# Kernel optimization log

Measured on AMD Instinct MI355X. Metric: run time of the kernel, lower is better.

Reference implementation:

```python
import jax, jax.numpy as jnp
import numpy as np

V, E, U, D, B, T = 32000, 256, 512, 512, 32, 64


def setup_inputs() -> dict:
    key = jax.random.key(0)
    ks = jax.random.split(key, 12)
    g = lambda k, shape: (jax.random.normal(k, shape, jnp.float32) * 0.05)
    return dict(
        x=jax.random.randint(ks[0], (B, T), 0, V),
        emb=g(ks[1], (V, E)),
        Wxf=g(ks[2], (E, 4 * U)), Whf=g(ks[3], (U, 4 * U)), bf=jnp.zeros((4 * U,), jnp.float32),
        Wxb=g(ks[4], (E, 4 * U)), Whb=g(ks[5], (U, 4 * U)), bb=jnp.zeros((4 * U,), jnp.float32),
        W1=g(ks[6], (2 * U + D, 10)), b1=jnp.zeros((10,), jnp.float32),
        W2=g(ks[7], (10, 1)), b2=jnp.zeros((1,), jnp.float32),
        Wxd=g(ks[8], (2 * U, 4 * D)), Whd=g(ks[9], (D, 4 * D)), bd=jnp.zeros((4 * D,), jnp.float32),
        Wo=g(ks[10], (D, V)), bo=jnp.zeros((V,), jnp.float32),
    )


def lstm_cell(x_t, h, c, Wx, Wh, b):
    # Keras gate order: i, f, g(cell), o
    z = x_t @ Wx + h @ Wh + b
    i, f, g, o = jnp.split(z, 4, axis=-1)
    c = jax.nn.sigmoid(f) * c + jax.nn.sigmoid(i) * jnp.tanh(g)
    h = jax.nn.sigmoid(o) * jnp.tanh(c)
    return h, c


def lstm_seq(xs, Wx, Wh, b):
    # xs: [T, B, F] -> hidden states [T, B, units]
    units = Wh.shape[0]
    h0 = jnp.zeros((xs.shape[1], units), xs.dtype)

    def step(carry, x_t):
        h, c = lstm_cell(x_t, carry[0], carry[1], Wx, Wh, b)
        return (h, c), h

    _, hs = jax.lax.scan(step, (h0, h0), xs)
    return hs


def reference(x, emb, Wxf, Whf, bf, Wxb, Whb, bb, W1, b1, W2, b2, Wxd, Whd, bd, Wo, bo):
    Bsz, Tlen = x.shape
    xe = emb[x]                              # [B, T, E]
    xs = jnp.swapaxes(xe, 0, 1)              # [T, B, E]
    hf = lstm_seq(xs, Wxf, Whf, bf)          # forward direction
    hb = lstm_seq(xs[::-1], Wxb, Whb, bb)[::-1]  # backward direction
    a = jnp.swapaxes(jnp.concatenate([hf, hb], axis=-1), 0, 1)  # [B, T, 2U]
    du = Whd.shape[0]

    def dec_step(carry, _):
        h, c = carry
        s_rep = jnp.broadcast_to(h[:, None, :], (Bsz, Tlen, du))
        cat = jnp.concatenate([a, s_rep], axis=-1)              # [B, T, 2U+D]
        e = jax.nn.relu(jnp.tanh(cat @ W1 + b1) @ W2 + b2)      # [B, T, 1]
        score = jax.nn.softmax(e, axis=1)
        ctx = jnp.sum(score * a, axis=1)                        # [B, 2U]
        h, c = lstm_cell(ctx, h, c, Wxd, Whd, bd)
        out = jax.nn.softmax(h @ Wo + bo, axis=-1)              # [B, V]
        return (h, c), out

    init = (jnp.zeros((Bsz, du), a.dtype), jnp.zeros((Bsz, du), a.dtype))
    _, outs = jax.lax.scan(dec_step, init, None, length=Tlen)
    return jnp.swapaxes(outs, 0, 1)  # [B, T, V]
```

## Files before the change

kernel.cpp:

```cpp
#include <hip/hip_runtime.h>
#include <hip/hip_bf16.h>
#include <cstdint>

typedef float f32x4 __attribute__((ext_vector_type(4)));
typedef __bf16 bf16x8 __attribute__((ext_vector_type(8)));

__device__ __forceinline__ uint32_t bf1(float x) {
  uint32_t u = __float_as_uint(x);
  return (u + 0x7fffu + ((u >> 16) & 1u)) >> 16;
}
__device__ __forceinline__ uint32_t bpack(float lo, float hi) {
  return bf1(lo) | (bf1(hi) << 16);
}
__device__ __forceinline__ float blo(uint32_t u) { return __uint_as_float(u << 16); }
__device__ __forceinline__ float bhi(uint32_t u) { return __uint_as_float(u & 0xffff0000u); }
__device__ __forceinline__ float sigm(float x) {
  return __fdividef(1.f, 1.f + exp2f(x * -1.4426950408889634f));
}
__device__ __forceinline__ float tanhf_fast(float x) {
  float e2 = exp2f(x * 2.8853900817779268f);
  return 1.f - __fdividef(2.f, e2 + 1.f);
}

__device__ __forceinline__ float dot2bf(uint32_t a, uint32_t b, float acc) {
  asm("v_dot2_f32_bf16 %0, %1, %2, %0" : "+v"(acc) : "v"(a), "v"(b));
  return acc;
}

#define GLOAD_LDS16(g, l)                                                     \
  __builtin_amdgcn_global_load_lds(                                           \
      (const __attribute__((address_space(1))) void*)(g),                     \
      (__attribute__((address_space(3))) void*)(l), 16, 0, 0)
#define GLOAD_LDS4(g, l)                                                      \
  __builtin_amdgcn_global_load_lds(                                           \
      (const __attribute__((address_space(1))) void*)(g),                     \
      (__attribute__((address_space(3))) void*)(l), 4, 0, 0)

__global__ __launch_bounds__(256) void k0_pack(
    const float* __restrict__ Whf, const float* __restrict__ Whb,
    uint32_t* __restrict__ Wencp, const float* __restrict__ Whd,
    uint32_t* __restrict__ Wdp, const float* __restrict__ W1,
    uint32_t* __restrict__ W1pbAll)
{
  int bid = blockIdx.x;
  if (bid < 4096) {
    int p = bid * 256 + threadIdx.x;
    int j2 = p & 3, slot = (p >> 2) & 63, c = (p >> 8) & 15;
    int cg = (p >> 12) & 127, dir = p >> 19;
    int k = slot * 8 + j2 * 2;
    const float* W = dir ? Whb : Whf;
    int colg = (c >> 2) * 512 + cg * 4 + (c & 3);
    Wencp[p ^ ((c & 7) << 2)] =
        bpack(W[(size_t)k * 2048 + colg], W[(size_t)(k + 1) * 2048 + colg]);
  } else if (bid < 6144) {
    int p = (bid - 4096) * 256 + threadIdx.x;
    int e = p & 3, cc = (p >> 2) & 31, q4 = (p >> 7) & 63, ug = p >> 13;
    int k2 = 4 * q4 + e;
    int col = (cc >> 3) * 512 + ug * 8 + (cc & 7);
    int k = 2 * k2;
    Wdp[p] = bpack(Whd[(size_t)k * 2048 + col], Whd[(size_t)(k + 1) * 2048 + col]);
  } else {
    int p = (bid - 6144) * 256 + threadIdx.x;
    if (p < 9216) {
      int q = p / 12, j = p % 12;
      float v0 = (j < 10) ? W1[(size_t)(2 * q) * 10 + j] : 0.f;
      float v1 = (j < 10) ? W1[(size_t)(2 * q + 1) * 10 + j] : 0.f;
      W1pbAll[p] = bpack(v0, v1);
    }
  }
}

__global__ __launch_bounds__(256) void k_wT(
    const float* __restrict__ src, ushort* __restrict__ dst, int K, int N)
{
  __shared__ float tile[64 * 65];
  const int t = threadIdx.x;
  const int n0 = blockIdx.x * 64, k0 = blockIdx.y * 64;
  for (int i = 0; i < 16; ++i) {
    int p = t + 256 * i;
    int kk = p >> 6, nn = p & 63;
    tile[kk * 65 + nn] = src[(size_t)(k0 + kk) * N + n0 + nn];
  }
  __syncthreads();
  for (int i = 0; i < 4; ++i) {
    int p = t + 256 * i;
    int nn = p >> 4, k4 = (p & 15) * 4;
    ushort4 o;
    o.x = (ushort)bf1(tile[(k4 + 0) * 65 + nn]);
    o.y = (ushort)bf1(tile[(k4 + 1) * 65 + nn]);
    o.z = (ushort)bf1(tile[(k4 + 2) * 65 + nn]);
    o.w = (ushort)bf1(tile[(k4 + 3) * 65 + nn]);
    *(ushort4*)(dst + (size_t)(n0 + nn) * K + k0 + k4) = o;
  }
}

__global__ __launch_bounds__(256) void k1_embed_mfma(
    const int* __restrict__ x, const float* __restrict__ emb,
    const ushort* __restrict__ WxfT, const ushort* __restrict__ WxbT,
    const float* __restrict__ bfv, const float* __restrict__ bbv,
    float* __restrict__ Xf, float* __restrict__ Xb)
{
  __shared__ float Afp[128 * 64];
  __shared__ ushort Bs[128 * 64];
  __shared__ int xid[128];
  const int t = threadIdx.x;
  const int n0g = blockIdx.x * 128;
  const int m0 = blockIdx.y * 128;
  const int isB = (n0g >= 2048);
  const int n0 = n0g & 2047;
  const ushort* WT = isB ? WxbT : WxfT;
  const float* bias = isB ? bbv : bfv;
  if (t < 128) xid[t] = x[m0 + t];
  __syncthreads();
  int xr[8];
#pragma unroll
  for (int i = 0; i < 8; ++i) xr[i] = xid[(t >> 4) + 16 * i];
  const int lane = t & 63, w = t >> 6;
  const int quad = lane >> 4, l15 = lane & 15;
  f32x4 acc[2][8] = {};
  for (int kc = 0; kc < 4; ++kc) {
    const int k0 = kc * 64;
    __syncthreads();
    for (int i = 0; i < 8; ++i) {
      int idx = t + 256 * i;
      int row = (t >> 4) + 16 * i, ch = idx & 15;
      int gr = (ch >> 1) ^ (row & 7), w16 = ch & 1;
      GLOAD_LDS16(emb + (size_t)xr[i] * 256 + k0 + gr * 8 + w16 * 4,
                  Afp + idx * 4);
    }
    for (int i = 0; i < 4; ++i) {
      int idx = t + 256 * i;
      int row = idx >> 3, s8 = (idx & 7) ^ (row & 7);
      GLOAD_LDS16(WT + (size_t)(n0 + row) * 256 + k0 + s8 * 8,
                  Bs + idx * 8);
    }
    __syncthreads();
#pragma unroll
    for (int ks = 0; ks < 2; ++ks) {
      int kq = ks * 4 + quad;
      bf16x8 af[2];
#pragma unroll
      for (int mi = 0; mi < 2; ++mi) {
        int row = w * 32 + mi * 16 + l15;
        int slot = kq ^ (row & 7);
        const float* ap = Afp + row * 64 + slot * 8;
        float4 a0 = *(const float4*)ap;
        float4 a1 = *(const float4*)(ap + 4);
        union { ushort u[8]; bf16x8 v; } cv;
        cv.u[0] = (ushort)bf1(a0.x); cv.u[1] = (ushort)bf1(a0.y);
        cv.u[2] = (ushort)bf1(a0.z); cv.u[3] = (ushort)bf1(a0.w);
        cv.u[4] = (ushort)bf1(a1.x); cv.u[5] = (ushort)bf1(a1.y);
        cv.u[6] = (ushort)bf1(a1.z); cv.u[7] = (ushort)bf1(a1.w);
        af[mi] = cv.v;
      }
#pragma unroll
      for (int ni = 0; ni < 8; ++ni) {
        int rowB = ni * 16 + l15;
        int slotB = kq ^ (rowB & 7);
        bf16x8 bfr = *(const bf16x8*)(Bs + rowB * 64 + slotB * 8);
#pragma unroll
        for (int mi = 0; mi < 2; ++mi)
          acc[mi][ni] = __builtin_amdgcn_mfma_f32_16x16x32_bf16(
              af[mi], bfr, acc[mi][ni], 0, 0, 0);
      }
    }
  }
  float* Xout = isB ? Xb : Xf;
  float bcol[8];
#pragma unroll
  for (int ni = 0; ni < 8; ++ni) bcol[ni] = bias[n0 + ni * 16 + l15];
#pragma unroll
  for (int mi = 0; mi < 2; ++mi) {
#pragma unroll
    for (int reg = 0; reg < 4; ++reg) {
      int token = m0 + w * 32 + mi * 16 + quad * 4 + reg;
#pragma unroll
      for (int ni = 0; ni < 8; ++ni) {
        int col = n0 + ni * 16 + l15;
        Xout[(size_t)token * 2048 + col] = acc[mi][ni][reg] + bcol[ni];
      }
    }
  }
}

__global__ __launch_bounds__(256) void k2_enc_step(
    const float* __restrict__ Xf, const float* __restrict__ Xb,
    const uint32_t* __restrict__ Wencp,
    const uint32_t* __restrict__ hfi, uint32_t* __restrict__ hfo,
    const uint32_t* __restrict__ hbi, uint32_t* __restrict__ hbo,
    float* __restrict__ cf, float* __restrict__ cb,
    ushort* __restrict__ aB, int step)
{
  __shared__ ushort Hs[16 * 512];
  __shared__ ushort Ws[16 * 512];
  __shared__ float zp[4 * 256];
  __shared__ float zx[256];
  __shared__ float zbuf[256];
  __shared__ float hl[64];
  const int t = threadIdx.x;
  const int dir = blockIdx.x >> 8;
  const int rh = (blockIdx.x >> 7) & 1;
  const int cg = blockIdx.x & 127;
  const int r0 = rh * 16, u0 = cg * 4;
  const float* XF = dir ? Xb : Xf;
  const uint32_t* hin = dir ? hbi : hfi;
  uint32_t* hout = dir ? hbo : hfo;
  float* cst = dir ? cb : cf;
  const int ta = dir ? (63 - step) : step;

  {
    const uint32_t* hinu = hin + r0 * 256;
    for (int i = 0; i < 4; ++i) {
      int b4 = (t >> 6) * 64 + 256 * i;
      GLOAD_LDS16(hinu + (size_t)(t + 256 * i) * 4, (uint32_t*)Hs + b4 * 4);
    }
    const uint32_t* wsrc = Wencp + ((size_t)dir * 128 + cg) * 4096;
    for (int i = 0; i < 4; ++i) {
      int b4 = (t >> 6) * 64 + 256 * i;
      GLOAD_LDS16(wsrc + (size_t)(t + 256 * i) * 4, (uint32_t*)Ws + b4 * 4);
    }
  }
  {
    int cl = t & 15, rl = t >> 4;
    int colg = (cl >> 2) * 512 + u0 + (cl & 3);
    GLOAD_LDS4(XF + (size_t)((r0 + rl) * 64 + ta) * 2048 + colg,
               zx + (t >> 6) * 64);
  }
  __syncthreads();
  const int lane = t & 63, w = t >> 6;
  const int quad = lane >> 4, l15 = lane & 15;
  f32x4 acc = {};
#pragma unroll
  for (int mm = 0; mm < 4; ++mm) {
    int m = w * 4 + mm;
    int slot = m * 4 + quad;
    bf16x8 a = *(const bf16x8*)(Hs + l15 * 512 + (slot ^ (l15 & 7)) * 8);
    bf16x8 b = *(const bf16x8*)(Ws + l15 * 512 + (slot ^ (l15 & 7)) * 8);
    acc = __builtin_amdgcn_mfma_f32_16x16x32_bf16(a, b, acc, 0, 0, 0);
  }
#pragma unroll
  for (int reg = 0; reg < 4; ++reg)
    zp[w * 256 + (quad * 4 + reg) * 16 + l15] = acc[reg];
  __syncthreads();
  zbuf[t] = zp[t] + zp[256 + t] + zp[512 + t] + zp[768 + t] + zx[t];
  __syncthreads();
  if (t < 64) {
    int rl = t & 15, ui = t >> 4;
    int u = u0 + ui, r = r0 + rl;
    float zi = zbuf[rl * 16 + ui];
    float zf = zbuf[rl * 16 + 4 + ui];
    float zg = zbuf[rl * 16 + 8 + ui];
    float zo = zbuf[rl * 16 + 12 + ui];
    float cold = cst[u * 32 + r];
    float cn = sigm(zf) * cold + sigm(zi) * tanhf_fast(zg);
    float h = sigm(zo) * tanhf_fast(cn);
    cst[u * 32 + r] = cn;
    aB[((size_t)r * 64 + ta) * 1024 + dir * 512 + u] = (ushort)bf1(h);
    hl[rl * 4 + ui] = h;
  }
  __syncthreads();
  if (t < 16) {
    int r = r0 + t;
    uint32_t lo = bpack(hl[t * 4 + 0], hl[t * 4 + 1]);
    uint32_t hi = bpack(hl[t * 4 + 2], hl[t * 4 + 3]);
    uint32_t* dst = hout + r * 256 + (((cg >> 1) ^ (r & 7)) * 4) + (cg & 1) * 2;
    *(uint2*)dst = make_uint2(lo, hi);
  }
}

__global__ __launch_bounds__(256) void k5_aw1(
    const ushort* __restrict__ aB, const uint32_t* __restrict__ W1pbAll,
    const float* __restrict__ b1, float* __restrict__ aw1)
{
  __shared__ uint32_t ar[512];
  __shared__ float ps[16 * 17];
  const int t = threadIdx.x;
  const uint32_t* aBu = (const uint32_t*)aB;
  for (int m = blockIdx.x; m < 2048; m += gridDim.x) {
    __syncthreads();
    *(uint2*)(&ar[t * 2]) = *(const uint2*)(aBu + (size_t)m * 512 + t * 2);
    __syncthreads();
    int j = t & 15, part = t >> 4;
    int jj = j < 10 ? j : 0;
    float s = 0.f;
#pragma unroll 8
    for (int q = part * 32; q < part * 32 + 32; ++q)
      s = dot2bf(ar[q], W1pbAll[q * 12 + jj], s);
    ps[part * 17 + j] = s;
    __syncthreads();
    if (t < 16) {
      float sum = 0.f;
      if (t < 10) {
        for (int p = 0; p < 16; ++p) sum += ps[p * 17 + t];
        sum += b1[t];
      }
      aw1[m * 16 + t] = sum;
    }
  }
}

__global__ __launch_bounds__(256) void kA_aprime(
    const ushort* __restrict__ WxdT, const ushort* __restrict__ aB,
    uint32_t* __restrict__ ApTb)
{
  __shared__ ushort As[128 * 64];
  __shared__ ushort Bs[128 * 64];
  const int t = threadIdx.x;
  const int lane = t & 63, w = t >> 6;
  const int wr = w >> 1, wc = w & 1;
  const int m0 = blockIdx.y * 128, n0 = blockIdx.x * 128;
  const int lrow = lane >> 3, s = lane & 7;
  const int quad = lane >> 4, l15 = lane & 15;
  f32x4 acc[4][4] = {};
  for (int kc = 0; kc < 16; ++kc) {
    const int k0 = kc * 64;
    __syncthreads();
    for (int i = 0; i < 4; ++i) {
      int row = w * 32 + i * 8 + lrow;
      int k8 = s ^ (row & 7);
      GLOAD_LDS16(WxdT + (size_t)(m0 + row) * 1024 + k0 + k8 * 8,
                  As + (w * 32 + i * 8) * 64);
      GLOAD_LDS16(aB + (size_t)(n0 + row) * 1024 + k0 + k8 * 8,
                  Bs + (w * 32 + i * 8) * 64);
    }
    __syncthreads();
#pragma unroll
    for (int ks = 0; ks < 2; ++ks) {
      bf16x8 af[4], bfr[4];
      int kq = ks * 4 + quad;
#pragma unroll
      for (int mi = 0; mi < 4; ++mi) {
        int row = wr * 64 + mi * 16 + l15;
        int slot = kq ^ (row & 7);
        af[mi] = *(const bf16x8*)(As + row * 64 + slot * 8);
      }
#pragma unroll
      for (int ni = 0; ni < 4; ++ni) {
        int row = wc * 64 + ni * 16 + l15;
        int slot = kq ^ (row & 7);
        bfr[ni] = *(const bf16x8*)(Bs + row * 64 + slot * 8);
      }
#pragma unroll
      for (int mi = 0; mi < 4; ++mi)
#pragma unroll
        for (int ni = 0; ni < 4; ++ni)
          acc[mi][ni] = __builtin_amdgcn_mfma_f32_16x16x32_bf16(
              af[mi], bfr[ni], acc[mi][ni], 0, 0, 0);
    }
  }
#pragma unroll
  for (int mi = 0; mi < 4; ++mi) {
    int mbase = m0 + wr * 64 + mi * 16 + quad * 4;
#pragma unroll
    for (int reg = 0; reg < 4; ++reg) {
      int m = mbase + reg;
#pragma unroll
      for (int ni = 0; ni < 4; ++ni) {
        int n = n0 + wc * 64 + ni * 16 + l15;
        float v = acc[mi][ni][reg];
        float v2 = __shfl_xor(v, 1);
        if (!(l15 & 1))
          ApTb[(size_t)m * 1024 + (n >> 1)] = bpack(v, v2);
      }
    }
  }
}

__global__ __launch_bounds__(256) void k4_dec_step(
    const uint32_t* __restrict__ ApTb, const float* __restrict__ aw1,
    const uint32_t* __restrict__ W1pb, const float* __restrict__ W2,
    const float* __restrict__ b2, const uint32_t* __restrict__ hdp_in,
    const uint32_t* __restrict__ Wdp, const float* __restrict__ bd,
    uint32_t* __restrict__ hdp_out, float* __restrict__ cd,
    ushort* __restrict__ HsB, int step)
{
  __shared__ uint32_t W1s[256 * 12];
  __shared__ uint32_t hdT[1024];
  __shared__ uint32_t Wsp[8192];
  __shared__ float ph[64 * 4 * 12];
  __shared__ float hw1[4 * 12];
  __shared__ float esc[4 * 65];
  __shared__ uint32_t escp[4 * 33];
  __shared__ float pm[4 * 9];
  __shared__ float mrow[4], srow[4];
  __shared__ float w2s[12];
  __shared__ float zp[2][128];
  __shared__ float zbuf[4 * 33];
  __shared__ float hl[32];
  const int t = threadIdx.x;
  const int ug = blockIdx.x >> 3;
  const int rg = blockIdx.x & 7;
  const int u0 = ug * 8, r0 = rg * 4;
  for (int i = 0; i < 3; ++i) {
    int b4 = (t >> 6) * 64 + 256 * i;
    GLOAD_LDS16(W1pb + (size_t)(t + 256 * i) * 4, W1s + (size_t)b4 * 4);
  }
  {
    int q4 = t >> 2, rl0 = t & 3;
    int b4 = (t >> 6) * 64;
    GLOAD_LDS16(hdp_in + (size_t)(q4 * 32 + r0 + rl0) * 4, hdT + (size_t)b4 * 4);
  }
  if (t < 12) w2s[t] = (t < 10) ? W2[t] : 0.f;
  __syncthreads();
  {
    const uint32_t* wsrc = Wdp + (size_t)ug * 8192;
    for (int i = 0; i < 8; ++i) {
      int b4 = (t >> 6) * 64 + 256 * i;
      GLOAD_LDS16(wsrc + (size_t)(t + 256 * i) * 4, Wsp + (size_t)b4 * 4);
    }
  }
  {
    const int rl = t & 3, kp = t >> 2;
    const uint4* hd4 = (const uint4*)hdT;
    float acc[10] = {};
    {
      uint4 u4 = hd4[kp * 4 + rl];
      const uint32_t* w0 = &W1s[(4 * kp) * 12];
      const uint32_t* w1 = &W1s[(4 * kp + 1) * 12];
      const uint32_t* w2p = &W1s[(4 * kp + 2) * 12];
      const uint32_t* w3 = &W1s[(4 * kp + 3) * 12];
#pragma unroll
      for (int j = 0; j < 10; ++j) {
        acc[j] = dot2bf(u4.x, w0[j], acc[j]);
        acc[j] = dot2bf(u4.y, w1[j], acc[j]);
        acc[j] = dot2bf(u4.z, w2p[j], acc[j]);
        acc[j] = dot2bf(u4.w, w3[j], acc[j]);
      }
    }
#pragma unroll
    for (int j = 0; j < 10; ++j) ph[(kp * 4 + rl) * 12 + j] = acc[j];
  }
  __syncthreads();
  if (t < 40) {
    int rl = t / 10, j = t % 10;
    float s = 0.f;
#pragma unroll
    for (int p = 0; p < 64; ++p) s += ph[(p * 4 + rl) * 12 + j];
    hw1[rl * 12 + j] = s;
  }
  __syncthreads();
  const float b2v = b2[0];
  {
    int rl = t >> 6, tt = t & 63;
    size_t m = (size_t)(r0 + rl) * 64 + tt;
    const float4* aw = (const float4*)(aw1 + m * 16);
    float4 q0 = aw[0], q1 = aw[1], q2 = aw[2];
    const float* hw = &hw1[rl * 12];
    float e = b2v;
    e += tanhf_fast(q0.x + hw[0]) * w2s[0];
    e += tanhf_fast(q0.y + hw[1]) * w2s[1];
    e += tanhf_fast(q0.z + hw[2]) * w2s[2];
    e += tanhf_fast(q0.w + hw[3]) * w2s[3];
    e += tanhf_fast(q1.x + hw[4]) * w2s[4];
    e += tanhf_fast(q1.y + hw[5]) * w2s[5];
    e += tanhf_fast(q1.z + hw[6]) * w2s[6];
    e += tanhf_fast(q1.w + hw[7]) * w2s[7];
    e += tanhf_fast(q2.x + hw[8]) * w2s[8];
    e += tanhf_fast(q2.y + hw[9]) * w2s[9];
    esc[rl * 65 + tt] = fmaxf(e, 0.f);
  }
  __syncthreads();
  if (t < 32) {
    int rl = t >> 3, part = t & 7;
    float m = -1e30f;
    for (int i = 0; i < 8; ++i) m = fmaxf(m, esc[rl * 65 + part * 8 + i]);
    pm[rl * 9 + part] = m;
  }
  __syncthreads();
  if (t < 4) {
    float m = pm[t * 9];
    for (int p = 1; p < 8; ++p) m = fmaxf(m, pm[t * 9 + p]);
    mrow[t] = m;
  }
  __syncthreads();
  if (t < 32) {
    int rl = t >> 3, part = t & 7;
    float m = mrow[rl];
    float s = 0.f;
    for (int i = 0; i < 8; ++i) s += __expf(esc[rl * 65 + part * 8 + i] - m);
    pm[rl * 9 + part] = s;
  }
  __syncthreads();
  if (t < 4) {
    float s = 0.f;
    for (int p = 0; p < 8; ++p) s += pm[t * 9 + p];
    srow[t] = __fdividef(1.f, s);
  }
  __syncthreads();
  if (t < 128) {
    int rl = t >> 5, q = t & 31;
    float m = mrow[rl], s = srow[rl];
    float v0 = __expf(esc[rl * 65 + 2 * q] - m) * s;
    float v1 = __expf(esc[rl * 65 + 2 * q + 1] - m) * s;
    escp[rl * 33 + q] = bpack(v0, v1);
  }
  __syncthreads();
  {
    const int out = t & 127;
    const int ccB = out >> 2, rl = out & 3;
    const int kh = t >> 7;
    const int colg = (ccB >> 3) * 512 + u0 + (ccB & 7);
    float acc = 0.f;
    {
      const uint4* hd4 = (const uint4*)hdT;
      const uint4* wd4 = (const uint4*)Wsp;
#pragma unroll 8
      for (int q4 = kh * 32; q4 < kh * 32 + 32; ++q4) {
        uint4 ua = hd4[q4 * 4 + rl];
        uint4 ub = wd4[q4 * 32 + ccB];
        acc = dot2bf(ua.x, ub.x, acc);
        acc = dot2bf(ua.y, ub.y, acc);
        acc = dot2bf(ua.z, ub.z, acc);
        acc = dot2bf(ua.w, ub.w, acc);
      }
    }
    {
      const uint32_t* ap = ApTb + (size_t)colg * 1024 + (r0 + rl) * 32;
      const uint32_t* ep = &escp[rl * 33];
#pragma unroll
      for (int i8 = kh * 4; i8 < kh * 4 + 4; ++i8) {
        uint4 v = *(const uint4*)(ap + i8 * 4);
        acc = dot2bf(v.x, ep[4 * i8 + 0], acc);
        acc = dot2bf(v.y, ep[4 * i8 + 1], acc);
        acc = dot2bf(v.z, ep[4 * i8 + 2], acc);
        acc = dot2bf(v.w, ep[4 * i8 + 3], acc);
      }
    }
    zp[kh][out] = acc;
  }
  __syncthreads();
  if (t < 128) {
    int ccB = t >> 2, rl = t & 3;
    int colg = (ccB >> 3) * 512 + u0 + (ccB & 7);
    zbuf[rl * 33 + ccB] = zp[0][t] + zp[1][t] + bd[colg];
  }
  __syncthreads();
  if (t < 32) {
    int j = t >> 2, rr = t & 3;
    int u = u0 + j, rgl = r0 + rr;
    float zi = zbuf[rr * 33 + j];
    float zf = zbuf[rr * 33 + 8 + j];
    float zg = zbuf[rr * 33 + 16 + j];
    float zo = zbuf[rr * 33 + 24 + j];
    float cold = cd[u * 32 + rgl];
    float cn = sigm(zf) * cold + sigm(zi) * tanhf_fast(zg);
    float h = sigm(zo) * tanhf_fast(cn);
    cd[u * 32 + rgl] = cn;
    HsB[(size_t)(step * 32 + rgl) * 512 + u] = (ushort)bf1(h);
    hl[j * 4 + rr] = h;
  }
  __syncthreads();
  if (t < 16) {
    int p = t >> 2, rr = t & 3;
    hdp_out[ug * 128 + (r0 + rr) * 4 + p] =
        bpack(hl[(2 * p) * 4 + rr], hl[(2 * p + 1) * 4 + rr]);
  }
}

__global__ __launch_bounds__(256) void k6_logits_mfma(
    const ushort* __restrict__ HsB, const ushort* __restrict__ WoT,
    const float* __restrict__ bo, float* __restrict__ out,
    float2* __restrict__ pstats, int moff)
{
  __shared__ ushort As[128 * 64];
  __shared__ ushort Bs[128 * 64];
  __shared__ float pm2[256], sm2[256];
  const int t = threadIdx.x;
  const int lane = t & 63, w = t >> 6;
  const int wr = w >> 1, wc = w & 1;
  const int m0 = (blockIdx.y + moff) * 128, n0 = blockIdx.x * 128;
  const int lrow = lane >> 3, s = lane & 7;
  const int quad = lane >> 4, l15 = lane & 15;
  f32x4 acc[4][4] = {};
  for (int kc = 0; kc < 8; ++kc) {
    const int k0 = kc * 64;
    __syncthreads();
    for (int i = 0; i < 4; ++i) {
      int row = w * 32 + i * 8 + lrow;
      int k8 = s ^ (row & 7);
      GLOAD_LDS16(HsB + (size_t)(m0 + row) * 512 + k0 + k8 * 8,
                  As + (w * 32 + i * 8) * 64);
      GLOAD_LDS16(WoT + (size_t)(n0 + row) * 512 + k0 + k8 * 8,
                  Bs + (w * 32 + i * 8) * 64);
    }
    __syncthreads();
#pragma unroll
    for (int ks = 0; ks < 2; ++ks) {
      bf16x8 af[4], bfr[4];
      int kq = ks * 4 + quad;
#pragma unroll
      for (int mi = 0; mi < 4; ++mi) {
        int row = wr * 64 + mi * 16 + l15;
        int slot = kq ^ (row & 7);
        af[mi] = *(const bf16x8*)(As + row * 64 + slot * 8);
      }
#pragma unroll
      for (int ni = 0; ni < 4; ++ni) {
        int row = wc * 64 + ni * 16 + l15;
        int slot = kq ^ (row & 7);
        bfr[ni] = *(const bf16x8*)(Bs + row * 64 + slot * 8);
      }
#pragma unroll
      for (int mi = 0; mi < 4; ++mi)
#pragma unroll
        for (int ni = 0; ni < 4; ++ni)
          acc[mi][ni] = __builtin_amdgcn_mfma_f32_16x16x32_bf16(
              af[mi], bfr[ni], acc[mi][ni], 0, 0, 0);
    }
  }
  __syncthreads();
  float* pmx = (float*)As;
  float* psm = (float*)Bs;
#pragma unroll
  for (int mi = 0; mi < 4; ++mi) {
    int mbase = m0 + wr * 64 + mi * 16 + quad * 4;
#pragma unroll
    for (int reg = 0; reg < 4; ++reg) {
      int m = mbase + reg;
      int rowl = (m - m0);
      size_t rowbase = ((size_t)(m & 31) * 64 + (m >> 5)) * 32000;
      float vs[4];
      float mx = -1e30f;
#pragma unroll
      for (int ni = 0; ni < 4; ++ni) {
        int n = n0 + wc * 64 + ni * 16 + l15;
        float v = acc[mi][ni][reg] + bo[n];
        out[rowbase + n] = v;
        vs[ni] = v;
        mx = fmaxf(mx, v);
      }
      float sl = __expf(vs[0] - mx) + __expf(vs[1] - mx) +
                 __expf(vs[2] - mx) + __expf(vs[3] - mx);
      pmx[rowl * 32 + wc * 16 + l15] = mx;
      psm[rowl * 32 + wc * 16 + l15] = sl;
    }
  }
  __syncthreads();
  {
    int rowl = t >> 1, hh = (t & 1) * 16;
    float m = pmx[rowl * 32 + hh], sacc = psm[rowl * 32 + hh];
    for (int i = 1; i < 16; ++i) {
      float m2 = pmx[rowl * 32 + hh + i], s2 = psm[rowl * 32 + hh + i];
      float mn = fmaxf(m, m2);
      sacc = sacc * __expf(m - mn) + s2 * __expf(m2 - mn);
      m = mn;
    }
    pm2[t] = m;
    sm2[t] = sacc;
  }
  __syncthreads();
  if (t < 128) {
    float m1 = pm2[2 * t], m2 = pm2[2 * t + 1];
    float mn = fmaxf(m1, m2);
    float sacc = sm2[2 * t] * __expf(m1 - mn) + sm2[2 * t + 1] * __expf(m2 - mn);
    int mg = m0 + t;
    int outrow = (mg & 31) * 64 + (mg >> 5);
    pstats[(size_t)outrow * 256 + blockIdx.x] = make_float2(mn, sacc);
  }
}

__global__ __launch_bounds__(256) void k7_softmax(
    float* __restrict__ out, const float2* __restrict__ pstats, int half)
{
  __shared__ float mred[256], sred[256];
  const int t = threadIdx.x;
  const int mg = half * 1024 + blockIdx.x;
  const int row = (mg & 31) * 64 + (mg >> 5);
  float m = -1e30f, s = 0.f;
  if (t < 250) {
    float2 p = pstats[(size_t)row * 256 + t];
    m = p.x;
    s = p.y;
  }
  mred[t] = m;
  sred[t] = s;
  __syncthreads();
  for (int st = 128; st > 0; st >>= 1) {
    if (t < st) {
      float m1 = mred[t], m2 = mred[t + st];
      float mn = fmaxf(m1, m2);
      sred[t] = sred[t] * __expf(m1 - mn) + sred[t + st] * __expf(m2 - mn);
      mred[t] = mn;
    }
    __syncthreads();
  }
  m = mred[0];
  const float inv = 1.f / sred[0];
  float* p = out + (size_t)row * 32000;
  for (int i = t; i < 8000; i += 256) {
    float4 v = *(const float4*)(p + i * 4);
    v.x = __expf(v.x - m) * inv;
    v.y = __expf(v.y - m) * inv;
    v.z = __expf(v.z - m) * inv;
    v.w = __expf(v.w - m) * inv;
    *(float4*)(p + i * 4) = v;
  }
}

extern "C" void kernel_launch(void* const* d_in, const int* in_sizes, int n_in,
                              void* d_out, int out_size, void* d_ws, size_t ws_size,
                              hipStream_t stream)
{
  const int* x = (const int*)d_in[0];
  const float* emb = (const float*)d_in[1];
  const float* Wxf = (const float*)d_in[2];
  const float* Whf = (const float*)d_in[3];
  const float* bfv = (const float*)d_in[4];
  const float* Wxb = (const float*)d_in[5];
  const float* Whb = (const float*)d_in[6];
  const float* bbv = (const float*)d_in[7];
  const float* W1 = (const float*)d_in[8];
  const float* b1 = (const float*)d_in[9];
  const float* W2 = (const float*)d_in[10];
  const float* b2 = (const float*)d_in[11];
  const float* Wxd = (const float*)d_in[12];
  const float* Whd = (const float*)d_in[13];
  const float* bd = (const float*)d_in[14];
  const float* Wo = (const float*)d_in[15];
  const float* bo = (const float*)d_in[16];

  float* ws = (float*)d_ws;
  float* c_f = ws + 0;
  float* c_b = ws + 16384;
  float* c_d = ws + 32768;
  uint32_t* hfp0 = (uint32_t*)(ws + 49152);
  uint32_t* hfp1 = hfp0 + 8192;
  uint32_t* hbp0 = (uint32_t*)(ws + 65536);
  uint32_t* hbp1 = hbp0 + 8192;
  uint32_t* hdp0 = (uint32_t*)(ws + 81920);
  uint32_t* hdp1 = hdp0 + 8192;
  uint32_t* W1pbAll = (uint32_t*)(ws + 98304);
  uint32_t* Wencp = (uint32_t*)(ws + 114688);
  uint32_t* Wdp = (uint32_t*)(ws + 1163264);
  ushort* aB = (ushort*)(ws + 1687552);
  float* aw1 = ws + 2742272;
  float* Xf = ws + 2775040;
  float* Xb = Xf + 4194304;
  ushort* WxfT = (ushort*)(ws + 11163648);
  ushort* WxbT = (ushort*)(ws + 11425792);
  ushort* HsB = (ushort*)(ws + 13260800);
  uint32_t* ApTb = (uint32_t*)Xf;
  ushort* WxdT = (ushort*)Xb;
  ushort* WoT = (ushort*)Xf;
  float2* pstats = (float2*)Wencp;

  hipMemsetAsync(ws, 0, 98304 * sizeof(float), stream);

  k0_pack<<<6180, 256, 0, stream>>>(Whf, Whb, Wencp, Whd, Wdp, W1, W1pbAll);
  k_wT<<<dim3(32, 4), 256, 0, stream>>>(Wxf, WxfT, 256, 2048);
  k_wT<<<dim3(32, 4), 256, 0, stream>>>(Wxb, WxbT, 256, 2048);

  k1_embed_mfma<<<dim3(32, 16), 256, 0, stream>>>(x, emb, WxfT, WxbT,
                                                  bfv, bbv, Xf, Xb);

  for (int s = 0; s < 64; ++s) {
    const uint32_t* hfi = (s & 1) ? hfp1 : hfp0;
    uint32_t* hfo = (s & 1) ? hfp0 : hfp1;
    const uint32_t* hbi = (s & 1) ? hbp1 : hbp0;
    uint32_t* hbo = (s & 1) ? hbp0 : hbp1;
    k2_enc_step<<<512, 256, 0, stream>>>(Xf, Xb, Wencp, hfi, hfo, hbi, hbo,
                                         c_f, c_b, aB, s);
  }

  k5_aw1<<<2048, 256, 0, stream>>>(aB, W1pbAll, b1, aw1);
  k_wT<<<dim3(32, 16), 256, 0, stream>>>(Wxd, WxdT, 1024, 2048);
  kA_aprime<<<dim3(16, 16), 256, 0, stream>>>(WxdT, aB, ApTb);

  for (int s = 0; s < 64; ++s) {
    const uint32_t* hdi = (s & 1) ? hdp1 : hdp0;
    uint32_t* hdo = (s & 1) ? hdp0 : hdp1;
    k4_dec_step<<<512, 256, 0, stream>>>(ApTb, aw1, W1pbAll + 6144, W2, b2,
                                         hdi, Wdp, bd, hdo, c_d, HsB, s);
  }

  k_wT<<<dim3(500, 8), 256, 0, stream>>>(Wo, WoT, 512, 32000);
  k6_logits_mfma<<<dim3(250, 8), 256, 0, stream>>>(HsB, WoT, bo,
                                                   (float*)d_out, pstats, 0);
  k7_softmax<<<1024, 256, 0, stream>>>((float*)d_out, pstats, 0);
  k6_logits_mfma<<<dim3(250, 8), 256, 0, stream>>>(HsB, WoT, bo,
                                                   (float*)d_out, pstats, 8);
  k7_softmax<<<1024, 256, 0, stream>>>((float*)d_out, pstats, 1);
}
```

Before: 1.457 ms.

## Merge Wx transposes, split decoder attention reduction, hoist output bias loads

Fuses the two separate forward/backward input-weight transpose launches into a single kernel with a doubled grid, saving one launch. In the decoder step kernel, the serial 64-term reduction done by 40 threads is split into a two-stage reduction over 160 threads, shortening the per-step critical path at the cost of an extra barrier. In the output projection epilogue, the bias values are loaded once per thread instead of inside the per-row loop.

```diff
diff --git a/kernel.cpp b/kernel.cpp
--- a/kernel.cpp
+++ b/kernel.cpp
@@ -94,6 +94,34 @@
   }
 }
 
+__global__ __launch_bounds__(256) void k_wTx(
+    const float* __restrict__ Wxf, ushort* __restrict__ WxfT,
+    const float* __restrict__ Wxb, ushort* __restrict__ WxbT)
+{
+  __shared__ float tile[64 * 65];
+  const int t = threadIdx.x;
+  const int ky = blockIdx.y;
+  const float* src = (ky < 4) ? Wxf : Wxb;
+  ushort* dst = (ky < 4) ? WxfT : WxbT;
+  const int n0 = blockIdx.x * 64, k0 = (ky & 3) * 64;
+  for (int i = 0; i < 16; ++i) {
+    int p = t + 256 * i;
+    int kk = p >> 6, nn = p & 63;
+    tile[kk * 65 + nn] = src[(size_t)(k0 + kk) * 2048 + n0 + nn];
+  }
+  __syncthreads();
+  for (int i = 0; i < 4; ++i) {
+    int p = t + 256 * i;
+    int nn = p >> 4, k4 = (p & 15) * 4;
+    ushort4 o;
+    o.x = (ushort)bf1(tile[(k4 + 0) * 65 + nn]);
+    o.y = (ushort)bf1(tile[(k4 + 1) * 65 + nn]);
+    o.z = (ushort)bf1(tile[(k4 + 2) * 65 + nn]);
+    o.w = (ushort)bf1(tile[(k4 + 3) * 65 + nn]);
+    *(ushort4*)(dst + (size_t)(n0 + nn) * 256 + k0 + k4) = o;
+  }
+}
+
 __global__ __launch_bounds__(256) void k1_embed_mfma(
     const int* __restrict__ x, const float* __restrict__ emb,
     const ushort* __restrict__ WxfT, const ushort* __restrict__ WxbT,
@@ -378,6 +406,7 @@
   __shared__ uint32_t hdT[1024];
   __shared__ uint32_t Wsp[8192];
   __shared__ float ph[64 * 4 * 12];
+  __shared__ float ph2[160];
   __shared__ float hw1[4 * 12];
   __shared__ float esc[4 * 65];
   __shared__ uint32_t escp[4 * 33];
@@ -431,12 +460,19 @@
     for (int j = 0; j < 10; ++j) ph[(kp * 4 + rl) * 12 + j] = acc[j];
   }
   __syncthreads();
+  if (t < 160) {
+    int g = t / 40, rem = t - g * 40;
+    int rl = rem / 10, j = rem % 10;
+    float s = 0.f;
+#pragma unroll
+    for (int p = 0; p < 16; ++p)
+      s += ph[((g * 16 + p) * 4 + rl) * 12 + j];
+    ph2[t] = s;
+  }
+  __syncthreads();
   if (t < 40) {
-    int rl = t / 10, j = t % 10;
-    float s = 0.f;
-#pragma unroll
-    for (int p = 0; p < 64; ++p) s += ph[(p * 4 + rl) * 12 + j];
-    hw1[rl * 12 + j] = s;
+    hw1[(t / 10) * 12 + (t % 10)] =
+        ph2[t] + ph2[40 + t] + ph2[80 + t] + ph2[120 + t];
   }
   __syncthreads();
   const float b2v = b2[0];
@@ -611,6 +647,10 @@
   __syncthreads();
   float* pmx = (float*)As;
   float* psm = (float*)Bs;
+  float bon[4];
+#pragma unroll
+  for (int ni = 0; ni < 4; ++ni)
+    bon[ni] = bo[n0 + wc * 64 + ni * 16 + l15];
 #pragma unroll
   for (int mi = 0; mi < 4; ++mi) {
     int mbase = m0 + wr * 64 + mi * 16 + quad * 4;
@@ -624,7 +664,7 @@
 #pragma unroll
       for (int ni = 0; ni < 4; ++ni) {
         int n = n0 + wc * 64 + ni * 16 + l15;
-        float v = acc[mi][ni][reg] + bo[n];
+        float v = acc[mi][ni][reg] + bon[ni];
         out[rowbase + n] = v;
         vs[ni] = v;
         mx = fmaxf(mx, v);
@@ -747,8 +787,7 @@
   hipMemsetAsync(ws, 0, 98304 * sizeof(float), stream);
 
   k0_pack<<<6180, 256, 0, stream>>>(Whf, Whb, Wencp, Whd, Wdp, W1, W1pbAll);
-  k_wT<<<dim3(32, 4), 256, 0, stream>>>(Wxf, WxfT, 256, 2048);
-  k_wT<<<dim3(32, 4), 256, 0, stream>>>(Wxb, WxbT, 256, 2048);
+  k_wTx<<<dim3(32, 8), 256, 0, stream>>>(Wxf, WxfT, Wxb, WxbT);
 
   k1_embed_mfma<<<dim3(32, 16), 256, 0, stream>>>(x, emb, WxfT, WxbT,
                                                   bfv, bbv, Xf, Xb);
```

Result: no change. 1.446 ms (-0.8%).
